# Performance work log

Hardware: AMD Instinct MI355X
Metric: run time of the kernel (lower is better)

The kernel has to match this reference:

```python
import jax, jax.numpy as jnp
import numpy as np

GRAPH_SIZE = 100   # nodes per graph (hardcoded reshape in Net.call)
CH = 64            # self.channel
BN_EPS = 1e-3      # keras BatchNormalization default epsilon

N_GRAPHS = 4096
N_NODES = N_GRAPHS * GRAPH_SIZE      # 409600
DEG = 16
N_EDGES = N_NODES * DEG              # 6,553,600


def setup_inputs() -> dict:
    key = jax.random.key(0)
    ks = jax.random.split(key, 12)
    x = jax.random.normal(ks[0], (N_NODES, CH), dtype=jnp.float32)
    # Edges confined within each 100-node graph block (disjoint-union batch).
    receivers = jax.random.randint(ks[1], (N_EDGES,), 0, N_NODES, dtype=jnp.int32)
    block = (receivers // GRAPH_SIZE) * GRAPH_SIZE
    senders = block + jax.random.randint(ks[2], (N_EDGES,), 0, GRAPH_SIZE, dtype=jnp.int32)
    s = lambda fan_in: 1.0 / np.sqrt(fan_in)
    return {
        "x": x,
        "senders": senders,
        "receivers": receivers,
        "W1": jax.random.normal(ks[3], (CH, CH), dtype=jnp.float32) * s(CH),
        "b1": jnp.zeros((CH,), jnp.float32),
        "gamma": jnp.ones((CH,), jnp.float32),
        "beta": jnp.zeros((CH,), jnp.float32),
        "bn_mean": jnp.zeros((CH,), jnp.float32),
        "bn_var": jnp.ones((CH,), jnp.float32),
        "W_d1": jax.random.normal(ks[4], (GRAPH_SIZE * CH, 256), dtype=jnp.float32) * s(GRAPH_SIZE * CH),
        "b_d1": jnp.zeros((256,), jnp.float32),
        "W_d2": jax.random.normal(ks[5], (256, 128), dtype=jnp.float32) * s(256),
        "b_d2": jnp.zeros((128,), jnp.float32),
        "W_d3": jax.random.normal(ks[6], (128, 1), dtype=jnp.float32) * s(128),
        "b_d3": jnp.zeros((1,), jnp.float32),
    }


def reference(x, senders, receivers, W1, b1, gamma, beta, bn_mean, bn_var,
              W_d1, b_d1, W_d2, b_d2, W_d3, b_d3):
    n = x.shape[0]
    # GeneralConv(aggregate='sum'): sum neighbor features, then linear+BN+ELU.
    agg = jax.ops.segment_sum(x[senders], receivers, num_segments=n)  # [N, CH]
    h = agg @ W1 + b1
    h = (h - bn_mean) * (gamma * jax.lax.rsqrt(bn_var + BN_EPS)) + beta
    h = jax.nn.elu(h)
    # reshape [N, CH] -> [N/100, 100*CH] (reshape + Flatten fused)
    h = h.reshape(n // GRAPH_SIZE, GRAPH_SIZE * CH)
    h = jax.nn.relu(h @ W_d1 + b_d1)
    h = jax.nn.relu(h @ W_d2 + b_d2)
    # dropout is identity at inference
    return jax.nn.sigmoid(h @ W_d3 + b_d3)  # [B, 1]
```

## Files before the change

kernel.cpp:

```cpp
#include <hip/hip_runtime.h>
#include <cstdint>
#include <cstddef>

#define GRAPH_SIZE 100
#define N_GRAPHS 4096
#define N_NODES (N_GRAPHS * GRAPH_SIZE)
#define DEG 16
#define N_EDGES (N_NODES * DEG)
#define BN_EPS 1e-3f

#define NB1 1024
#define NPB 400
#define PCHUNK 12800
#define NPWG (N_EDGES / PCHUNK)
#define BSTRIDE 8192
#define ECAP 2304

typedef __attribute__((ext_vector_type(8))) unsigned short ushort8;
typedef __attribute__((ext_vector_type(8))) short short8;
typedef __attribute__((ext_vector_type(4))) float f32x4;

__device__ __forceinline__ unsigned f2bf(float f) {
  unsigned u = __float_as_uint(f);
  return (u + 0x7FFFu + ((u >> 16) & 1u)) >> 16;
}
__device__ __forceinline__ float bf2f(unsigned h) {
  return __uint_as_float(h << 16);
}

__global__ __launch_bounds__(256) void count1_kernel(const int* __restrict__ recv,
                                                     unsigned* __restrict__ wg_hist) {
  __shared__ unsigned lh[NB1];
  int tid = threadIdx.x, w = blockIdx.x;
  for (int i = tid; i < NB1; i += 256) lh[i] = 0;
  __syncthreads();
  size_t base = (size_t)w * PCHUNK;
  for (int i = tid; i < PCHUNK; i += 256)
    atomicAdd(&lh[(unsigned)recv[base + i] / NPB], 1u);
  __syncthreads();
  for (int i = tid; i < NB1; i += 256) wg_hist[(size_t)w * NB1 + i] = lh[i];
}

__global__ __launch_bounds__(256) void scan_wg_kernel(unsigned* __restrict__ wg_hist,
                                                      unsigned* __restrict__ gtotal) {
  int b = blockIdx.x * 256 + threadIdx.x;
  unsigned run = 0;
  for (int w = 0; w < NPWG; w++) {
    size_t idx = (size_t)w * NB1 + b;
    unsigned c = wg_hist[idx];
    wg_hist[idx] = run;
    run += c;
  }
  gtotal[b] = run;
}

__global__ __launch_bounds__(256) void scan_bucket_kernel(const unsigned* __restrict__ gtotal,
                                                          unsigned* __restrict__ gbase) {
  __shared__ unsigned tmp[256];
  int tid = threadIdx.x;
  unsigned my[4], s4 = 0;
#pragma unroll
  for (int j = 0; j < 4; j++) { my[j] = gtotal[tid * 4 + j]; s4 += my[j]; }
  tmp[tid] = s4;
  __syncthreads();
  unsigned acc = s4;
  for (int d = 1; d < 256; d <<= 1) {
    unsigned t = (tid >= d) ? tmp[tid - d] : 0;
    __syncthreads();
    acc += t;
    tmp[tid] = acc;
    __syncthreads();
  }
  unsigned run = tmp[tid] - s4;
#pragma unroll
  for (int j = 0; j < 4; j++) { gbase[tid * 4 + j] = run; run += my[j]; }
}

__global__ __launch_bounds__(256) void partition1_kernel(const int* __restrict__ recv,
                                                         const int* __restrict__ send,
                                                         const unsigned* __restrict__ wg_hist,
                                                         const unsigned* __restrict__ gbase,
                                                         unsigned short* __restrict__ midrec) {
  __shared__ unsigned cur[NB1];
  __shared__ unsigned tmp[256];
  __shared__ unsigned stage[PCHUNK];
  int tid = threadIdx.x, w = blockIdx.x;
  size_t base = (size_t)w * PCHUNK;

  for (int i = tid; i < NB1; i += 256) cur[i] = 0;
  __syncthreads();
  for (int i = tid; i < PCHUNK; i += 256)
    atomicAdd(&cur[(unsigned)recv[base + i] / NPB], 1u);
  __syncthreads();

  unsigned my[4], s4 = 0;
#pragma unroll
  for (int j = 0; j < 4; j++) { my[j] = cur[tid * 4 + j]; s4 += my[j]; }
  tmp[tid] = s4;
  __syncthreads();
  unsigned acc = s4;
  for (int d = 1; d < 256; d <<= 1) {
    unsigned t = (tid >= d) ? tmp[tid - d] : 0;
    __syncthreads();
    acc += t;
    tmp[tid] = acc;
    __syncthreads();
  }
  unsigned run = tmp[tid] - s4;
#pragma unroll
  for (int j = 0; j < 4; j++) { cur[tid * 4 + j] = run; run += my[j]; }
  __syncthreads();

  for (int i = tid; i < PCHUNK; i += 256) {
    unsigned r = (unsigned)recv[base + i];
    unsigned s = (unsigned)send[base + i];
    unsigned b = r / NPB;
    unsigned rin = r - b * NPB;
    unsigned gib = rin / 100;
    unsigned rl = rin - gib * 100;
    unsigned sl = s - (s / 100) * 100;
    unsigned pos = atomicAdd(&cur[b], 1u);
    stage[pos] = (b << 16) | (gib << 14) | (sl << 7) | rl;
  }
  __syncthreads();

  const unsigned* wrow = wg_hist + (size_t)w * NB1;
  for (int p = tid; p < PCHUNK; p += 256) {
    unsigned rec = stage[p];
    unsigned b = rec >> 16;
    unsigned start = (b > 0) ? cur[b - 1] : 0;
    unsigned dest = gbase[b] + wrow[b] + ((unsigned)p - start);
    midrec[dest] = (unsigned short)(rec & 0xFFFFu);
  }
}

__global__ __launch_bounds__(256) void sort2_kernel(const unsigned short* __restrict__ midrec,
                                                    const unsigned* __restrict__ gtotal,
                                                    const unsigned* __restrict__ gbase,
                                                    unsigned short* __restrict__ sorted,
                                                    unsigned* __restrict__ noff) {
  __shared__ unsigned short smid[BSTRIDE];
  __shared__ unsigned short dst[BSTRIDE];
  __shared__ unsigned hist[512];
  __shared__ unsigned tmp[256];
  __shared__ unsigned s_ptot;
  int tid = threadIdx.x, b = blockIdx.x;
  unsigned cnt = gtotal[b];
  if (cnt > BSTRIDE) cnt = BSTRIDE;
  unsigned gb = gbase[b];

  for (unsigned i = tid; i < cnt; i += 256) smid[i] = midrec[gb + i];
  hist[tid] = 0; hist[256 + tid] = 0;
  {
    unsigned* d32 = (unsigned*)dst;
    for (int i = tid; i < BSTRIDE / 2; i += 256) d32[i] = 0x19001900u;
  }
  __syncthreads();

  for (unsigned i = tid; i < cnt; i += 256) {
    unsigned rec = smid[i];
    unsigned nib = (rec >> 14) * 100 + (rec & 127u);
    atomicAdd(&hist[nib], 1u);
  }
  __syncthreads();

  unsigned c0 = hist[2 * tid], c1 = hist[2 * tid + 1];
  unsigned p0 = (c0 + 3u) & ~3u, p1 = (c1 + 3u) & ~3u;
  unsigned s2 = p0 + p1;
  tmp[tid] = s2;
  __syncthreads();
  unsigned acc = s2;
  for (int d = 1; d < 256; d <<= 1) {
    unsigned t = (tid >= d) ? tmp[tid - d] : 0;
    __syncthreads();
    acc += t;
    tmp[tid] = acc;
    __syncthreads();
  }
  unsigned pb0 = acc - s2;
  unsigned pb1 = pb0 + p0;
  unsigned obase = (unsigned)b * BSTRIDE;
  int k0 = 2 * tid, k1 = 2 * tid + 1;
  if (k0 <= NPB) noff[(size_t)b * 401 + k0] = obase + pb0;
  if (k1 <= NPB) noff[(size_t)b * 401 + k1] = obase + pb1;
  if (k0 == NPB) s_ptot = pb0;
  __syncthreads();
  hist[k0] = pb0;
  hist[k1] = pb1;
  __syncthreads();

  for (unsigned i = tid; i < cnt; i += 256) {
    unsigned rec = smid[i];
    unsigned nib = (rec >> 14) * 100 + (rec & 127u);
    unsigned pos = atomicAdd(&hist[nib], 1u);
    if (pos < BSTRIDE) dst[pos] = (unsigned short)(((rec >> 7) & 127u) * 64u);
  }
  __syncthreads();

  unsigned ptot = s_ptot;
  if (ptot > BSTRIDE) ptot = BSTRIDE;
  unsigned* o32 = (unsigned*)sorted + (size_t)b * (BSTRIDE / 2);
  unsigned* d32 = (unsigned*)dst;
  for (unsigned i = tid; i < (ptot >> 1); i += 256) o32[i] = d32[i];
}

__global__ __launch_bounds__(256) void aggconv_kernel(
    const float* __restrict__ x, const unsigned* __restrict__ noff,
    const unsigned short* __restrict__ sorted,
    const float* __restrict__ W1, const float* __restrict__ b1,
    const float* __restrict__ gamma, const float* __restrict__ beta,
    const float* __restrict__ bn_mean, const float* __restrict__ bn_var,
    unsigned short* __restrict__ h_hi, unsigned short* __restrict__ h_lo) {
  __shared__ float xs[6464];
  __shared__ unsigned short es[ECAP];
  __shared__ unsigned nof[104];
  int tid = threadIdx.x, lane = tid & 63, wv = tid >> 6;
  int g = blockIdx.x;
  size_t gb64 = (size_t)g * 6400;

  const float4* xsrc = (const float4*)(x + gb64);
  float4* xd = (float4*)xs;
  for (int i = tid; i < 1600; i += 256) xd[i] = xsrc[i];
  if (tid < 64) xs[6400 + tid] = 0.f;

  int b = g >> 2, gib = g & 3;
  size_t base401 = (size_t)b * 401 + (size_t)gib * 100;
  unsigned gbeg = noff[base401];
  unsigned gend = noff[base401 + 100];
  unsigned ecnt = gend - gbeg;
  if (ecnt > ECAP) ecnt = ECAP;
  if (tid <= 100) nof[tid] = noff[base401 + tid] - gbeg;
  {
    const unsigned* s32 = (const unsigned*)sorted + (gbeg >> 1);
    unsigned* e32 = (unsigned*)es;
    for (unsigned i = tid; i < (ecnt >> 1); i += 256) e32[i] = s32[i];
  }
  __syncthreads();

  float accs[25];
#pragma unroll
  for (int J = 0; J < 25; J++) {
    int n = wv + 4 * J;
    unsigned e = nof[n], e1 = nof[n + 1];
    float acc = 0.f;
    for (; e < e1; e += 4) {
      unsigned long long v = *(const unsigned long long*)&es[e];
      acc += xs[((unsigned)v & 0xFFFFu) + lane];
      acc += xs[((unsigned)(v >> 16) & 0xFFFFu) + lane];
      acc += xs[((unsigned)(v >> 32) & 0xFFFFu) + lane];
      acc += xs[(unsigned)(v >> 48) + lane];
    }
    accs[J] = acc;
  }
  __syncthreads();
#pragma unroll
  for (int J = 0; J < 25; J++) xs[(wv + 4 * J) * 64 + lane] = accs[J];
  __syncthreads();

  float w[64];
#pragma unroll
  for (int i = 0; i < 64; i++) w[i] = W1[i * 64 + lane];
  float scale = gamma[lane] * rsqrtf(bn_var[lane] + BN_EPS);
  float mb = bn_mean[lane], bt = beta[lane], bias1 = b1[lane];

#pragma unroll
  for (int J = 0; J < 25; J++) {
    int n = wv + 4 * J;
    float hv = bias1;
#pragma unroll
    for (int q = 0; q < 16; q++) {
      float4 av = *(const float4*)&xs[n * 64 + q * 4];
      hv = fmaf(av.x, w[q * 4 + 0], hv);
      hv = fmaf(av.y, w[q * 4 + 1], hv);
      hv = fmaf(av.z, w[q * 4 + 2], hv);
      hv = fmaf(av.w, w[q * 4 + 3], hv);
    }
    hv = (hv - mb) * scale + bt;
    hv = (hv > 0.f) ? hv : expm1f(hv);
    unsigned hi = f2bf(hv);
    unsigned lo = f2bf(hv - bf2f(hi));
    size_t idx = gb64 + (size_t)n * 64 + lane;
    h_hi[idx] = (unsigned short)hi;
    h_lo[idx] = (unsigned short)lo;
  }
}

__global__ __launch_bounds__(256) void wcvt_kernel(const float* __restrict__ W,
                                                   unsigned short* __restrict__ Bhi,
                                                   unsigned short* __restrict__ Blo) {
  __shared__ float sm[64][65];
  int tid = threadIdx.x;
  int k0 = blockIdx.x * 64;
  int n0 = blockIdx.y * 64;
  for (int i = tid; i < 1024; i += 256) {
    int r = i >> 4, c4 = i & 15;
    float4 v = *(const float4*)&W[(size_t)(k0 + r) * 256 + n0 + c4 * 4];
    sm[r][c4 * 4 + 0] = v.x; sm[r][c4 * 4 + 1] = v.y;
    sm[r][c4 * 4 + 2] = v.z; sm[r][c4 * 4 + 3] = v.w;
  }
  __syncthreads();
  for (int i = tid; i < 512; i += 256) {
    int nn = i >> 3, kk = i & 7;
    ushort8 hi, lo;
#pragma unroll
    for (int j = 0; j < 8; j++) {
      float f = sm[kk * 8 + j][nn];
      unsigned hb = f2bf(f);
      hi[j] = (unsigned short)hb;
      lo[j] = (unsigned short)f2bf(f - bf2f(hb));
    }
    size_t o = (size_t)(n0 + nn) * 6400 + k0 + kk * 8;
    *(ushort8*)&Bhi[o] = hi;
    *(ushort8*)&Blo[o] = lo;
  }
}

#define G2_SPLIT 8
#define G2_KSLICE 800
#define G2_STEPS (G2_KSLICE / 32)
__global__ __launch_bounds__(256) void gemm2_kernel(const unsigned short* __restrict__ Ahi,
                                                    const unsigned short* __restrict__ Alo,
                                                    const unsigned short* __restrict__ Bhi,
                                                    const unsigned short* __restrict__ Blo,
                                                    float* __restrict__ Cp) {
  __shared__ __align__(16) unsigned short As[2][64 * 40];
  __shared__ __align__(16) unsigned short Bs[2][256 * 40];
  int tid = threadIdx.x;
  int w = tid >> 6, l = tid & 63;
  int bm = blockIdx.x * 64;
  int kslice = blockIdx.y * G2_KSLICE;

  f32x4 acc[4][4];
#pragma unroll
  for (int i = 0; i < 4; i++)
#pragma unroll
    for (int j = 0; j < 4; j++) acc[i][j] = (f32x4){0.f, 0.f, 0.f, 0.f};

  int arow = tid >> 2, akg = tid & 3;
  const size_t abase = (size_t)(bm + arow) * 6400 + kslice + akg * 8;

  ushort8 pa_hi, pa_lo, pb_hi[4], pb_lo[4];
  pa_hi = *(const ushort8*)&Ahi[abase];
  pa_lo = *(const ushort8*)&Alo[abase];
#pragma unroll
  for (int i = 0; i < 4; i++) {
    int u = tid + 256 * i;
    size_t bb = (size_t)(u >> 2) * 6400 + kslice + (u & 3) * 8;
    pb_hi[i] = *(const ushort8*)&Bhi[bb];
    pb_lo[i] = *(const ushort8*)&Blo[bb];
  }

  for (int step = 0; step < G2_STEPS; step++) {
    __syncthreads();
    *(ushort8*)&As[0][arow * 40 + akg * 8] = pa_hi;
    *(ushort8*)&As[1][arow * 40 + akg * 8] = pa_lo;
#pragma unroll
    for (int i = 0; i < 4; i++) {
      int u = tid + 256 * i;
      *(ushort8*)&Bs[0][(u >> 2) * 40 + (u & 3) * 8] = pb_hi[i];
      *(ushort8*)&Bs[1][(u >> 2) * 40 + (u & 3) * 8] = pb_lo[i];
    }
    __syncthreads();

    if (step + 1 < G2_STEPS) {
      size_t koff = (size_t)(step + 1) * 32;
      pa_hi = *(const ushort8*)&Ahi[abase + koff];
      pa_lo = *(const ushort8*)&Alo[abase + koff];
#pragma unroll
      for (int i = 0; i < 4; i++) {
        int u = tid + 256 * i;
        size_t bb = (size_t)(u >> 2) * 6400 + kslice + (u & 3) * 8 + koff;
        pb_hi[i] = *(const ushort8*)&Bhi[bb];
        pb_lo[i] = *(const ushort8*)&Blo[bb];
      }
    }

    int kg8 = (l >> 4) * 8;
    short8 a_hi[4], a_lo[4];
#pragma unroll
    for (int mf = 0; mf < 4; mf++) {
      int r = mf * 16 + (l & 15);
      a_hi[mf] = *(const short8*)&As[0][r * 40 + kg8];
      a_lo[mf] = *(const short8*)&As[1][r * 40 + kg8];
    }
#pragma unroll
    for (int nf = 0; nf < 4; nf++) {
      int c = w * 64 + nf * 16 + (l & 15);
      short8 b_hi = *(const short8*)&Bs[0][c * 40 + kg8];
      short8 b_lo = *(const short8*)&Bs[1][c * 40 + kg8];
#pragma unroll
      for (int mf = 0; mf < 4; mf++) {
        acc[mf][nf] = __builtin_amdgcn_mfma_f32_16x16x32_bf16(a_hi[mf], b_hi, acc[mf][nf], 0, 0, 0);
        acc[mf][nf] = __builtin_amdgcn_mfma_f32_16x16x32_bf16(a_hi[mf], b_lo, acc[mf][nf], 0, 0, 0);
        acc[mf][nf] = __builtin_amdgcn_mfma_f32_16x16x32_bf16(a_lo[mf], b_hi, acc[mf][nf], 0, 0, 0);
      }
    }
  }

  float* outp = Cp + (size_t)blockIdx.y * N_GRAPHS * 256;
#pragma unroll
  for (int mf = 0; mf < 4; mf++)
#pragma unroll
    for (int nf = 0; nf < 4; nf++)
#pragma unroll
      for (int r = 0; r < 4; r++)
        outp[(size_t)(bm + mf * 16 + (l >> 4) * 4 + r) * 256 + w * 64 + nf * 16 + (l & 15)] =
            acc[mf][nf][r];
}

__global__ __launch_bounds__(256) void reduce_kernel(const float* __restrict__ Cp,
                                                     const float* __restrict__ bias,
                                                     float* __restrict__ out1) {
  int i = blockIdx.x * 256 + threadIdx.x;
  const size_t S = (size_t)N_GRAPHS * 256;
  float v = bias[i & 255];
#pragma unroll
  for (int s = 0; s < G2_SPLIT; s++) v += Cp[s * S + i];
  out1[i] = fmaxf(v, 0.f);
}

__global__ __launch_bounds__(256) void tail_kernel(const float* __restrict__ out1,
                                                   const float* __restrict__ Wd2,
                                                   const float* __restrict__ bd2,
                                                   const float* __restrict__ Wd3,
                                                   const float* __restrict__ bd3,
                                                   float* __restrict__ out) {
  int lane = threadIdx.x & 63;
  int wave = threadIdx.x >> 6;
  int row = blockIdx.x * 4 + wave;

  const float* in = out1 + (size_t)row * 256;
  float i0 = in[lane];
  float i1 = in[64 + lane];
  float i2 = in[128 + lane];
  float i3 = in[192 + lane];

  float a0 = bd2[lane];
  float a1 = bd2[64 + lane];
#pragma unroll
  for (int i = 0; i < 64; i++) {
    float v0 = __shfl(i0, i);
    a0 = fmaf(v0, Wd2[(i)*128 + lane], a0);
    a1 = fmaf(v0, Wd2[(i)*128 + 64 + lane], a1);
    float v1 = __shfl(i1, i);
    a0 = fmaf(v1, Wd2[(64 + i) * 128 + lane], a0);
    a1 = fmaf(v1, Wd2[(64 + i) * 128 + 64 + lane], a1);
    float v2 = __shfl(i2, i);
    a0 = fmaf(v2, Wd2[(128 + i) * 128 + lane], a0);
    a1 = fmaf(v2, Wd2[(128 + i) * 128 + 64 + lane], a1);
    float v3 = __shfl(i3, i);
    a0 = fmaf(v3, Wd2[(192 + i) * 128 + lane], a0);
    a1 = fmaf(v3, Wd2[(192 + i) * 128 + 64 + lane], a1);
  }
  a0 = fmaxf(a0, 0.f);
  a1 = fmaxf(a1, 0.f);
  float p = a0 * Wd3[lane] + a1 * Wd3[64 + lane];
#pragma unroll
  for (int m = 32; m >= 1; m >>= 1) p += __shfl_xor(p, m);
  if (lane == 0) out[row] = 1.f / (1.f + expf(-(p + bd3[0])));
}

extern "C" void kernel_launch(void* const* d_in, const int* in_sizes, int n_in,
                              void* d_out, int out_size, void* d_ws, size_t ws_size,
                              hipStream_t stream) {
  const float* x        = (const float*)d_in[0];
  const int*   senders  = (const int*)d_in[1];
  const int*   receivers= (const int*)d_in[2];
  const float* W1       = (const float*)d_in[3];
  const float* b1       = (const float*)d_in[4];
  const float* gamma    = (const float*)d_in[5];
  const float* beta     = (const float*)d_in[6];
  const float* bn_mean  = (const float*)d_in[7];
  const float* bn_var   = (const float*)d_in[8];
  const float* W_d1     = (const float*)d_in[9];
  const float* b_d1     = (const float*)d_in[10];
  const float* W_d2     = (const float*)d_in[11];
  const float* b_d2     = (const float*)d_in[12];
  const float* W_d3     = (const float*)d_in[13];
  const float* b_d3     = (const float*)d_in[14];
  float* out = (float*)d_out;

  char* ws = (char*)d_ws;
  unsigned short* h_hi = (unsigned short*)ws; ws += (size_t)N_NODES * 64 * 2;
  unsigned short* h_lo = (unsigned short*)ws; ws += (size_t)N_NODES * 64 * 2;
  char* regB = ws;                       ws += (size_t)NPWG * NB1 * 4;
  unsigned* wg_hist = (unsigned*)regB;
  unsigned* noff    = (unsigned*)regB;
  unsigned* gtotal  = (unsigned*)ws;     ws += NB1 * 4;
  unsigned* gbase   = (unsigned*)ws;     ws += NB1 * 4;
  unsigned short* Bt_hi = (unsigned short*)ws; ws += (size_t)256 * 6400 * 2;
  unsigned short* Bt_lo = (unsigned short*)ws; ws += (size_t)256 * 6400 * 2;
  char* regDE = ws;
  unsigned short* midrec = (unsigned short*)regDE;
  unsigned short* sorted = (unsigned short*)(regDE + (size_t)N_EDGES * 2);
  float* Cp   = (float*)regDE;
  float* out1 = (float*)(regDE + (size_t)G2_SPLIT * N_GRAPHS * 256 * 4);

  count1_kernel<<<NPWG, 256, 0, stream>>>(receivers, wg_hist);
  scan_wg_kernel<<<NB1 / 256, 256, 0, stream>>>(wg_hist, gtotal);
  scan_bucket_kernel<<<1, 256, 0, stream>>>(gtotal, gbase);
  partition1_kernel<<<NPWG, 256, 0, stream>>>(receivers, senders, wg_hist, gbase, midrec);
  sort2_kernel<<<NB1, 256, 0, stream>>>(midrec, gtotal, gbase, sorted, noff);
  wcvt_kernel<<<dim3(100, 4), 256, 0, stream>>>(W_d1, Bt_hi, Bt_lo);
  aggconv_kernel<<<N_GRAPHS, 256, 0, stream>>>(x, noff, sorted, W1, b1,
                                               gamma, beta, bn_mean, bn_var, h_hi, h_lo);
  gemm2_kernel<<<dim3(N_GRAPHS / 64, G2_SPLIT), 256, 0, stream>>>(h_hi, h_lo, Bt_hi, Bt_lo, Cp);
  reduce_kernel<<<(N_GRAPHS * 256) / 256, 256, 0, stream>>>(Cp, b_d1, out1);
  tail_kernel<<<N_GRAPHS / 4, 256, 0, stream>>>(out1, W_d2, b_d2, W_d3, b_d3, out);
}
```

Before: 514.4 us.

## Replace two-level edge sort with per-graph adjacency count matrix and MFMA aggregation

Partitions edges directly into one bucket per graph, dropping the second sort pass and the global bucket scan. Each graph's aggregation becomes a dense 100x100 adjacency-count matrix built with shared-memory atomics. That matrix is multiplied by the node features on bf16 MFMA, using hi/lo splits to keep near-fp32 accuracy, followed by a second MFMA GEMM with W1 that is pre-converted once. The aim is to cut sorting passes and scalar gather work, at the cost of a fixed 2048-edge cap per graph and heavier shared-memory use.

```diff
diff --git a/kernel.cpp b/kernel.cpp
--- a/kernel.cpp
+++ b/kernel.cpp
@@ -9,12 +9,10 @@
 #define N_EDGES (N_NODES * DEG)
 #define BN_EPS 1e-3f
 
-#define NB1 1024
-#define NPB 400
+#define NB 4096
 #define PCHUNK 12800
 #define NPWG (N_EDGES / PCHUNK)
-#define BSTRIDE 8192
-#define ECAP 2304
+#define ESTRIDE 2048
 
 typedef __attribute__((ext_vector_type(8))) unsigned short ushort8;
 typedef __attribute__((ext_vector_type(8))) short short8;
@@ -27,18 +25,26 @@
 __device__ __forceinline__ float bf2f(unsigned h) {
   return __uint_as_float(h << 16);
 }
+__device__ __forceinline__ short8 cvt8(float4 a, float4 b) {
+  short8 r;
+  r[0] = (short)f2bf(a.x); r[1] = (short)f2bf(a.y);
+  r[2] = (short)f2bf(a.z); r[3] = (short)f2bf(a.w);
+  r[4] = (short)f2bf(b.x); r[5] = (short)f2bf(b.y);
+  r[6] = (short)f2bf(b.z); r[7] = (short)f2bf(b.w);
+  return r;
+}
 
 __global__ __launch_bounds__(256) void count1_kernel(const int* __restrict__ recv,
                                                      unsigned* __restrict__ wg_hist) {
-  __shared__ unsigned lh[NB1];
+  __shared__ unsigned lh[NB];
   int tid = threadIdx.x, w = blockIdx.x;
-  for (int i = tid; i < NB1; i += 256) lh[i] = 0;
+  for (int i = tid; i < NB; i += 256) lh[i] = 0;
   __syncthreads();
   size_t base = (size_t)w * PCHUNK;
   for (int i = tid; i < PCHUNK; i += 256)
-    atomicAdd(&lh[(unsigned)recv[base + i] / NPB], 1u);
-  __syncthreads();
-  for (int i = tid; i < NB1; i += 256) wg_hist[(size_t)w * NB1 + i] = lh[i];
+    atomicAdd(&lh[(unsigned)recv[base + i] / GRAPH_SIZE], 1u);
+  __syncthreads();
+  for (int i = tid; i < NB; i += 256) wg_hist[(size_t)w * NB + i] = lh[i];
 }
 
 __global__ __launch_bounds__(256) void scan_wg_kernel(unsigned* __restrict__ wg_hist,
@@ -46,7 +52,7 @@
   int b = blockIdx.x * 256 + threadIdx.x;
   unsigned run = 0;
   for (int w = 0; w < NPWG; w++) {
-    size_t idx = (size_t)w * NB1 + b;
+    size_t idx = (size_t)w * NB + b;
     unsigned c = wg_hist[idx];
     wg_hist[idx] = run;
     run += c;
@@ -54,16 +60,29 @@
   gtotal[b] = run;
 }
 
-__global__ __launch_bounds__(256) void scan_bucket_kernel(const unsigned* __restrict__ gtotal,
-                                                          unsigned* __restrict__ gbase) {
+__global__ __launch_bounds__(256) void partition1_kernel(const int* __restrict__ recv,
+                                                         const int* __restrict__ send,
+                                                         const unsigned* __restrict__ wg_hist,
+                                                         unsigned short* __restrict__ edges) {
+  __shared__ unsigned cur[NB];
   __shared__ unsigned tmp[256];
+  __shared__ unsigned stage[PCHUNK];
   int tid = threadIdx.x;
-  unsigned my[4], s4 = 0;
-#pragma unroll
-  for (int j = 0; j < 4; j++) { my[j] = gtotal[tid * 4 + j]; s4 += my[j]; }
-  tmp[tid] = s4;
-  __syncthreads();
-  unsigned acc = s4;
+  int w = (blockIdx.x & 7) * (NPWG / 8) + (blockIdx.x >> 3);
+  size_t base = (size_t)w * PCHUNK;
+
+  for (int i = tid; i < NB; i += 256) cur[i] = 0;
+  __syncthreads();
+  for (int i = tid; i < PCHUNK; i += 256)
+    atomicAdd(&cur[(unsigned)recv[base + i] / GRAPH_SIZE], 1u);
+  __syncthreads();
+
+  unsigned my[16], s16 = 0;
+#pragma unroll
+  for (int j = 0; j < 16; j++) { my[j] = cur[tid * 16 + j]; s16 += my[j]; }
+  tmp[tid] = s16;
+  __syncthreads();
+  unsigned acc = s16;
   for (int d = 1; d < 256; d <<= 1) {
     unsigned t = (tid >= d) ? tmp[tid - d] : 0;
     __syncthreads();
@@ -71,218 +90,213 @@
     tmp[tid] = acc;
     __syncthreads();
   }
-  unsigned run = tmp[tid] - s4;
-#pragma unroll
-  for (int j = 0; j < 4; j++) { gbase[tid * 4 + j] = run; run += my[j]; }
-}
-
-__global__ __launch_bounds__(256) void partition1_kernel(const int* __restrict__ recv,
-                                                         const int* __restrict__ send,
-                                                         const unsigned* __restrict__ wg_hist,
-                                                         const unsigned* __restrict__ gbase,
-                                                         unsigned short* __restrict__ midrec) {
-  __shared__ unsigned cur[NB1];
-  __shared__ unsigned tmp[256];
-  __shared__ unsigned stage[PCHUNK];
-  int tid = threadIdx.x, w = blockIdx.x;
-  size_t base = (size_t)w * PCHUNK;
-
-  for (int i = tid; i < NB1; i += 256) cur[i] = 0;
-  __syncthreads();
-  for (int i = tid; i < PCHUNK; i += 256)
-    atomicAdd(&cur[(unsigned)recv[base + i] / NPB], 1u);
-  __syncthreads();
-
-  unsigned my[4], s4 = 0;
-#pragma unroll
-  for (int j = 0; j < 4; j++) { my[j] = cur[tid * 4 + j]; s4 += my[j]; }
-  tmp[tid] = s4;
-  __syncthreads();
-  unsigned acc = s4;
-  for (int d = 1; d < 256; d <<= 1) {
-    unsigned t = (tid >= d) ? tmp[tid - d] : 0;
-    __syncthreads();
-    acc += t;
-    tmp[tid] = acc;
-    __syncthreads();
-  }
-  unsigned run = tmp[tid] - s4;
-#pragma unroll
-  for (int j = 0; j < 4; j++) { cur[tid * 4 + j] = run; run += my[j]; }
+  unsigned run = acc - s16;
+#pragma unroll
+  for (int j = 0; j < 16; j++) { cur[tid * 16 + j] = run; run += my[j]; }
   __syncthreads();
 
   for (int i = tid; i < PCHUNK; i += 256) {
     unsigned r = (unsigned)recv[base + i];
     unsigned s = (unsigned)send[base + i];
-    unsigned b = r / NPB;
-    unsigned rin = r - b * NPB;
-    unsigned gib = rin / 100;
-    unsigned rl = rin - gib * 100;
-    unsigned sl = s - (s / 100) * 100;
-    unsigned pos = atomicAdd(&cur[b], 1u);
-    stage[pos] = (b << 16) | (gib << 14) | (sl << 7) | rl;
-  }
-  __syncthreads();
-
-  const unsigned* wrow = wg_hist + (size_t)w * NB1;
+    unsigned g = r / GRAPH_SIZE;
+    unsigned rl = r - g * GRAPH_SIZE;
+    unsigned sl = s - (s / GRAPH_SIZE) * GRAPH_SIZE;
+    unsigned pos = atomicAdd(&cur[g], 1u);
+    stage[pos] = (g << 16) | (sl << 7) | rl;
+  }
+  __syncthreads();
+
+  const unsigned* wrow = wg_hist + (size_t)w * NB;
   for (int p = tid; p < PCHUNK; p += 256) {
     unsigned rec = stage[p];
-    unsigned b = rec >> 16;
-    unsigned start = (b > 0) ? cur[b - 1] : 0;
-    unsigned dest = gbase[b] + wrow[b] + ((unsigned)p - start);
-    midrec[dest] = (unsigned short)(rec & 0xFFFFu);
-  }
-}
-
-__global__ __launch_bounds__(256) void sort2_kernel(const unsigned short* __restrict__ midrec,
-                                                    const unsigned* __restrict__ gtotal,
-                                                    const unsigned* __restrict__ gbase,
-                                                    unsigned short* __restrict__ sorted,
-                                                    unsigned* __restrict__ noff) {
-  __shared__ unsigned short smid[BSTRIDE];
-  __shared__ unsigned short dst[BSTRIDE];
-  __shared__ unsigned hist[512];
-  __shared__ unsigned tmp[256];
-  __shared__ unsigned s_ptot;
-  int tid = threadIdx.x, b = blockIdx.x;
-  unsigned cnt = gtotal[b];
-  if (cnt > BSTRIDE) cnt = BSTRIDE;
-  unsigned gb = gbase[b];
-
-  for (unsigned i = tid; i < cnt; i += 256) smid[i] = midrec[gb + i];
-  hist[tid] = 0; hist[256 + tid] = 0;
-  {
-    unsigned* d32 = (unsigned*)dst;
-    for (int i = tid; i < BSTRIDE / 2; i += 256) d32[i] = 0x19001900u;
-  }
-  __syncthreads();
-
-  for (unsigned i = tid; i < cnt; i += 256) {
-    unsigned rec = smid[i];
-    unsigned nib = (rec >> 14) * 100 + (rec & 127u);
-    atomicAdd(&hist[nib], 1u);
-  }
-  __syncthreads();
-
-  unsigned c0 = hist[2 * tid], c1 = hist[2 * tid + 1];
-  unsigned p0 = (c0 + 3u) & ~3u, p1 = (c1 + 3u) & ~3u;
-  unsigned s2 = p0 + p1;
-  tmp[tid] = s2;
-  __syncthreads();
-  unsigned acc = s2;
-  for (int d = 1; d < 256; d <<= 1) {
-    unsigned t = (tid >= d) ? tmp[tid - d] : 0;
-    __syncthreads();
-    acc += t;
-    tmp[tid] = acc;
-    __syncthreads();
-  }
-  unsigned pb0 = acc - s2;
-  unsigned pb1 = pb0 + p0;
-  unsigned obase = (unsigned)b * BSTRIDE;
-  int k0 = 2 * tid, k1 = 2 * tid + 1;
-  if (k0 <= NPB) noff[(size_t)b * 401 + k0] = obase + pb0;
-  if (k1 <= NPB) noff[(size_t)b * 401 + k1] = obase + pb1;
-  if (k0 == NPB) s_ptot = pb0;
-  __syncthreads();
-  hist[k0] = pb0;
-  hist[k1] = pb1;
-  __syncthreads();
-
-  for (unsigned i = tid; i < cnt; i += 256) {
-    unsigned rec = smid[i];
-    unsigned nib = (rec >> 14) * 100 + (rec & 127u);
-    unsigned pos = atomicAdd(&hist[nib], 1u);
-    if (pos < BSTRIDE) dst[pos] = (unsigned short)(((rec >> 7) & 127u) * 64u);
-  }
-  __syncthreads();
-
-  unsigned ptot = s_ptot;
-  if (ptot > BSTRIDE) ptot = BSTRIDE;
-  unsigned* o32 = (unsigned*)sorted + (size_t)b * (BSTRIDE / 2);
-  unsigned* d32 = (unsigned*)dst;
-  for (unsigned i = tid; i < (ptot >> 1); i += 256) o32[i] = d32[i];
+    unsigned g = rec >> 16;
+    unsigned start = (g > 0) ? cur[g - 1] : 0;
+    unsigned local = wrow[g] + ((unsigned)p - start);
+    if (local < ESTRIDE)
+      edges[(size_t)g * ESTRIDE + local] = (unsigned short)(rec & 0x3FFFu);
+  }
+}
+
+__global__ __launch_bounds__(256) void w1cvt_kernel(const float* __restrict__ W1,
+                                                    unsigned short* __restrict__ Whi,
+                                                    unsigned short* __restrict__ Wlo) {
+  int tid = threadIdx.x;
+  for (int idx = tid; idx < 4096; idx += 256) {
+    int o = idx >> 6, i = idx & 63;
+    float f = W1[i * 64 + o];
+    unsigned hb = f2bf(f);
+    Whi[o * 64 + i] = (unsigned short)hb;
+    Wlo[o * 64 + i] = (unsigned short)f2bf(f - bf2f(hb));
+  }
 }
 
 __global__ __launch_bounds__(256) void aggconv_kernel(
-    const float* __restrict__ x, const unsigned* __restrict__ noff,
-    const unsigned short* __restrict__ sorted,
-    const float* __restrict__ W1, const float* __restrict__ b1,
-    const float* __restrict__ gamma, const float* __restrict__ beta,
-    const float* __restrict__ bn_mean, const float* __restrict__ bn_var,
+    const float* __restrict__ x, const unsigned* __restrict__ gtotal,
+    const unsigned short* __restrict__ edges,
+    const unsigned short* __restrict__ W1t_hi, const unsigned short* __restrict__ W1t_lo,
+    const float* __restrict__ b1, const float* __restrict__ gamma,
+    const float* __restrict__ beta, const float* __restrict__ bn_mean,
+    const float* __restrict__ bn_var,
     unsigned short* __restrict__ h_hi, unsigned short* __restrict__ h_lo) {
-  __shared__ float xs[6464];
-  __shared__ unsigned short es[ECAP];
-  __shared__ unsigned nof[104];
+  __shared__ __align__(16) float S[100 * 104];
+  __shared__ __align__(16) unsigned short Xhi[64 * 104];
+  __shared__ __align__(16) unsigned short Xlo[64 * 104];
+  __shared__ __align__(16) unsigned short es_s[ESTRIDE];
+  __shared__ float prm[128];
+  __shared__ __align__(16) unsigned short zslot[16];
+
   int tid = threadIdx.x, lane = tid & 63, wv = tid >> 6;
+  int l15 = lane & 15, hg = lane >> 4;
   int g = blockIdx.x;
   size_t gb64 = (size_t)g * 6400;
 
-  const float4* xsrc = (const float4*)(x + gb64);
-  float4* xd = (float4*)xs;
-  for (int i = tid; i < 1600; i += 256) xd[i] = xsrc[i];
-  if (tid < 64) xs[6400 + tid] = 0.f;
-
-  int b = g >> 2, gib = g & 3;
-  size_t base401 = (size_t)b * 401 + (size_t)gib * 100;
-  unsigned gbeg = noff[base401];
-  unsigned gend = noff[base401 + 100];
-  unsigned ecnt = gend - gbeg;
-  if (ecnt > ECAP) ecnt = ECAP;
-  if (tid <= 100) nof[tid] = noff[base401 + tid] - gbeg;
+  short8 wfh[4][2], wfl[4][2];
+#pragma unroll
+  for (int nf = 0; nf < 4; nf++)
+#pragma unroll
+    for (int ks = 0; ks < 2; ks++) {
+      int o = nf * 16 + l15, k = ks * 32 + hg * 8;
+      wfh[nf][ks] = *(const short8*)&W1t_hi[o * 64 + k];
+      wfl[nf][ks] = *(const short8*)&W1t_lo[o * 64 + k];
+    }
+
   {
-    const unsigned* s32 = (const unsigned*)sorted + (gbeg >> 1);
-    unsigned* e32 = (unsigned*)es;
-    for (unsigned i = tid; i < (ecnt >> 1); i += 256) e32[i] = s32[i];
-  }
-  __syncthreads();
-
-  float accs[25];
-#pragma unroll
-  for (int J = 0; J < 25; J++) {
-    int n = wv + 4 * J;
-    unsigned e = nof[n], e1 = nof[n + 1];
-    float acc = 0.f;
-    for (; e < e1; e += 4) {
-      unsigned long long v = *(const unsigned long long*)&es[e];
-      acc += xs[((unsigned)v & 0xFFFFu) + lane];
-      acc += xs[((unsigned)(v >> 16) & 0xFFFFu) + lane];
-      acc += xs[((unsigned)(v >> 32) & 0xFFFFu) + lane];
-      acc += xs[(unsigned)(v >> 48) + lane];
-    }
-    accs[J] = acc;
-  }
-  __syncthreads();
-#pragma unroll
-  for (int J = 0; J < 25; J++) xs[(wv + 4 * J) * 64 + lane] = accs[J];
-  __syncthreads();
-
-  float w[64];
-#pragma unroll
-  for (int i = 0; i < 64; i++) w[i] = W1[i * 64 + lane];
-  float scale = gamma[lane] * rsqrtf(bn_var[lane] + BN_EPS);
-  float mb = bn_mean[lane], bt = beta[lane], bias1 = b1[lane];
-
-#pragma unroll
-  for (int J = 0; J < 25; J++) {
-    int n = wv + 4 * J;
-    float hv = bias1;
-#pragma unroll
-    for (int q = 0; q < 16; q++) {
-      float4 av = *(const float4*)&xs[n * 64 + q * 4];
-      hv = fmaf(av.x, w[q * 4 + 0], hv);
-      hv = fmaf(av.y, w[q * 4 + 1], hv);
-      hv = fmaf(av.z, w[q * 4 + 2], hv);
-      hv = fmaf(av.w, w[q * 4 + 3], hv);
-    }
-    hv = (hv - mb) * scale + bt;
-    hv = (hv > 0.f) ? hv : expm1f(hv);
-    unsigned hi = f2bf(hv);
-    unsigned lo = f2bf(hv - bf2f(hi));
-    size_t idx = gb64 + (size_t)n * 64 + lane;
-    h_hi[idx] = (unsigned short)hi;
-    h_lo[idx] = (unsigned short)lo;
-  }
+    float4 z4 = {0.f, 0.f, 0.f, 0.f};
+    float4* S4 = (float4*)S;
+    for (int i = tid; i < 2600; i += 256) S4[i] = z4;
+  }
+#pragma unroll
+  for (int j = 0; j < 25; j++) {
+    int i = tid + 256 * j;
+    float v = x[gb64 + i];
+    int node = i >> 6, ch = i & 63;
+    unsigned hb = f2bf(v);
+    Xhi[ch * 104 + node] = (unsigned short)hb;
+    Xlo[ch * 104 + node] = (unsigned short)f2bf(v - bf2f(hb));
+  }
+  if (tid < 64) {
+#pragma unroll
+    for (int c = 100; c < 104; c++) { Xhi[tid * 104 + c] = 0; Xlo[tid * 104 + c] = 0; }
+    float sc = gamma[tid] * rsqrtf(bn_var[tid] + BN_EPS);
+    prm[tid] = sc;
+    prm[64 + tid] = (b1[tid] - bn_mean[tid]) * sc + beta[tid];
+  }
+  if (tid < 16) zslot[tid] = 0;
+  unsigned cnt = gtotal[g];
+  if (cnt > ESTRIDE) cnt = ESTRIDE;
+  {
+    const unsigned* e32 = (const unsigned*)(edges + (size_t)g * ESTRIDE);
+    unsigned* d32 = (unsigned*)es_s;
+    unsigned n32 = (cnt + 1) >> 1;
+    for (unsigned i = tid; i < n32; i += 256) d32[i] = e32[i];
+  }
+  __syncthreads();
+
+  for (unsigned e = tid; e < cnt; e += 256) {
+    unsigned rec = es_s[e];
+    atomicAdd(&S[(rec & 127u) * 104 + (rec >> 7)], 1.0f);
+  }
+  __syncthreads();
+
+  int mts[2];
+  mts[0] = wv;
+  mts[1] = (wv < 3) ? 4 + wv : 6;
+  f32x4 acc1[2][4];
+#pragma unroll
+  for (int mi = 0; mi < 2; mi++)
+#pragma unroll
+    for (int nf = 0; nf < 4; nf++) acc1[mi][nf] = (f32x4){0.f, 0.f, 0.f, 0.f};
+
+#pragma unroll
+  for (int ks = 0; ks < 4; ks++) {
+    int k0 = ks * 32 + hg * 8;
+    bool kv = (k0 <= 96);
+    short8 bh[4], bl[4];
+#pragma unroll
+    for (int nf = 0; nf < 4; nf++) {
+      int col = nf * 16 + l15;
+      const unsigned short* ph = kv ? &Xhi[col * 104 + k0] : zslot;
+      const unsigned short* pl = kv ? &Xlo[col * 104 + k0] : zslot;
+      bh[nf] = *(const short8*)ph;
+      bl[nf] = *(const short8*)pl;
+    }
+#pragma unroll
+    for (int mi = 0; mi < 2; mi++) {
+      int row = mts[mi] * 16 + l15;
+      const float* ap = kv ? &S[row * 104 + k0] : (const float*)zslot;
+      float4 a0 = *(const float4*)ap;
+      float4 a1 = *(const float4*)(ap + 4);
+      short8 af = cvt8(a0, a1);
+#pragma unroll
+      for (int nf = 0; nf < 4; nf++) {
+        acc1[mi][nf] = __builtin_amdgcn_mfma_f32_16x16x32_bf16(af, bh[nf], acc1[mi][nf], 0, 0, 0);
+        acc1[mi][nf] = __builtin_amdgcn_mfma_f32_16x16x32_bf16(af, bl[nf], acc1[mi][nf], 0, 0, 0);
+      }
+    }
+  }
+  __syncthreads();
+
+  unsigned short* Ahi = (unsigned short*)S;
+  unsigned short* Alo = Ahi + 112 * 72;
+#pragma unroll
+  for (int mi = 0; mi < 2; mi++)
+#pragma unroll
+    for (int nf = 0; nf < 4; nf++)
+#pragma unroll
+      for (int r = 0; r < 4; r++) {
+        float v = acc1[mi][nf][r];
+        int m = mts[mi] * 16 + hg * 4 + r;
+        int kc = nf * 16 + l15;
+        unsigned hb = f2bf(v);
+        Ahi[m * 72 + kc] = (unsigned short)hb;
+        Alo[m * 72 + kc] = (unsigned short)f2bf(v - bf2f(hb));
+      }
+  __syncthreads();
+
+  f32x4 acc2[2][4];
+#pragma unroll
+  for (int mi = 0; mi < 2; mi++)
+#pragma unroll
+    for (int nf = 0; nf < 4; nf++) acc2[mi][nf] = (f32x4){0.f, 0.f, 0.f, 0.f};
+#pragma unroll
+  for (int ks = 0; ks < 2; ks++) {
+    int k0 = ks * 32 + hg * 8;
+#pragma unroll
+    for (int mi = 0; mi < 2; mi++) {
+      int row = mts[mi] * 16 + l15;
+      short8 ah = *(const short8*)&Ahi[row * 72 + k0];
+      short8 al = *(const short8*)&Alo[row * 72 + k0];
+#pragma unroll
+      for (int nf = 0; nf < 4; nf++) {
+        acc2[mi][nf] = __builtin_amdgcn_mfma_f32_16x16x32_bf16(ah, wfh[nf][ks], acc2[mi][nf], 0, 0, 0);
+        acc2[mi][nf] = __builtin_amdgcn_mfma_f32_16x16x32_bf16(ah, wfl[nf][ks], acc2[mi][nf], 0, 0, 0);
+        acc2[mi][nf] = __builtin_amdgcn_mfma_f32_16x16x32_bf16(al, wfh[nf][ks], acc2[mi][nf], 0, 0, 0);
+      }
+    }
+  }
+
+  float scv[4], shv[4];
+#pragma unroll
+  for (int nf = 0; nf < 4; nf++) {
+    scv[nf] = prm[nf * 16 + l15];
+    shv[nf] = prm[64 + nf * 16 + l15];
+  }
+#pragma unroll
+  for (int mi = 0; mi < 2; mi++)
+#pragma unroll
+    for (int nf = 0; nf < 4; nf++)
+#pragma unroll
+      for (int r = 0; r < 4; r++) {
+        int node = mts[mi] * 16 + hg * 4 + r;
+        if (node < 100) {
+          float v = fmaf(acc2[mi][nf][r], scv[nf], shv[nf]);
+          v = (v > 0.f) ? v : (__expf(v) - 1.f);
+          unsigned hb = f2bf(v);
+          size_t idx = gb64 + (size_t)node * 64 + nf * 16 + l15;
+          h_hi[idx] = (unsigned short)hb;
+          h_lo[idx] = (unsigned short)f2bf(v - bf2f(hb));
+        }
+      }
 }
 
 __global__ __launch_bounds__(256) void wcvt_kernel(const float* __restrict__ W,
@@ -483,27 +497,24 @@
   char* ws = (char*)d_ws;
   unsigned short* h_hi = (unsigned short*)ws; ws += (size_t)N_NODES * 64 * 2;
   unsigned short* h_lo = (unsigned short*)ws; ws += (size_t)N_NODES * 64 * 2;
-  char* regB = ws;                       ws += (size_t)NPWG * NB1 * 4;
-  unsigned* wg_hist = (unsigned*)regB;
-  unsigned* noff    = (unsigned*)regB;
-  unsigned* gtotal  = (unsigned*)ws;     ws += NB1 * 4;
-  unsigned* gbase   = (unsigned*)ws;     ws += NB1 * 4;
+  unsigned* gtotal = (unsigned*)ws;           ws += NB * 4;
   unsigned short* Bt_hi = (unsigned short*)ws; ws += (size_t)256 * 6400 * 2;
   unsigned short* Bt_lo = (unsigned short*)ws; ws += (size_t)256 * 6400 * 2;
-  char* regDE = ws;
-  unsigned short* midrec = (unsigned short*)regDE;
-  unsigned short* sorted = (unsigned short*)(regDE + (size_t)N_EDGES * 2);
-  float* Cp   = (float*)regDE;
-  float* out1 = (float*)(regDE + (size_t)G2_SPLIT * N_GRAPHS * 256 * 4);
+  unsigned short* W1t_hi = (unsigned short*)ws; ws += 4096 * 2;
+  unsigned short* W1t_lo = (unsigned short*)ws; ws += 4096 * 2;
+  char* region = ws;
+  unsigned* wg_hist = (unsigned*)region;
+  unsigned short* edges = (unsigned short*)(region + (size_t)NPWG * NB * 4);
+  float* Cp   = (float*)region;
+  float* out1 = (float*)(region + (size_t)G2_SPLIT * N_GRAPHS * 256 * 4);
 
   count1_kernel<<<NPWG, 256, 0, stream>>>(receivers, wg_hist);
-  scan_wg_kernel<<<NB1 / 256, 256, 0, stream>>>(wg_hist, gtotal);
-  scan_bucket_kernel<<<1, 256, 0, stream>>>(gtotal, gbase);
-  partition1_kernel<<<NPWG, 256, 0, stream>>>(receivers, senders, wg_hist, gbase, midrec);
-  sort2_kernel<<<NB1, 256, 0, stream>>>(midrec, gtotal, gbase, sorted, noff);
+  scan_wg_kernel<<<NB / 256, 256, 0, stream>>>(wg_hist, gtotal);
+  partition1_kernel<<<NPWG, 256, 0, stream>>>(receivers, senders, wg_hist, edges);
+  w1cvt_kernel<<<1, 256, 0, stream>>>(W1, W1t_hi, W1t_lo);
   wcvt_kernel<<<dim3(100, 4), 256, 0, stream>>>(W_d1, Bt_hi, Bt_lo);
-  aggconv_kernel<<<N_GRAPHS, 256, 0, stream>>>(x, noff, sorted, W1, b1,
-                                               gamma, beta, bn_mean, bn_var, h_hi, h_lo);
+  aggconv_kernel<<<N_GRAPHS, 256, 0, stream>>>(x, gtotal, edges, W1t_hi, W1t_lo,
+                                               b1, gamma, beta, bn_mean, bn_var, h_hi, h_lo);
   gemm2_kernel<<<dim3(N_GRAPHS / 64, G2_SPLIT), 256, 0, stream>>>(h_hi, h_lo, Bt_hi, Bt_lo, Cp);
   reduce_kernel<<<(N_GRAPHS * 256) / 256, 256, 0, stream>>>(Cp, b_d1, out1);
   tail_kernel<<<N_GRAPHS / 4, 256, 0, stream>>>(out1, W_d2, b_d2, W_d3, b_d3, out);
```

After: 511.5 us. About the same (-0.6%).
